# Optimization experiments

Measured on AMD Instinct MI355X. Metric: run time of the kernel, lower is better.

Reference implementation:

```python
import jax, jax.numpy as jnp
import numpy as np

B, N_ANG, LX, LY, LZ = 2, 120, 128, 128, 128


def _rotate_z(vol, phi):
    """Rotate vol [B,Lx,Ly,Lz] by phi radians (counterclockwise) in the (x,y)
    plane about the grid center, bilinear interpolation, zero padding.
    Mirrors pytomography's rotate_detector_z (bilinear grid-sample rotate)."""
    Lx, Ly = vol.shape[1], vol.shape[2]
    dt = vol.dtype
    cx = (Lx - 1) / 2.0
    cy = (Ly - 1) / 2.0
    xs = jnp.arange(Lx, dtype=dt) - cx
    ys = jnp.arange(Ly, dtype=dt) - cy
    X, Y = jnp.meshgrid(xs, ys, indexing="ij")  # [Lx,Ly]
    c, s = jnp.cos(phi), jnp.sin(phi)
    # inverse rotation maps each output pixel to its source location
    sx = c * X + s * Y + cx
    sy = -s * X + c * Y + cy
    x0 = jnp.floor(sx)
    y0 = jnp.floor(sy)
    wx = (sx - x0)[None, :, :, None]
    wy = (sy - y0)[None, :, :, None]
    x0i = x0.astype(jnp.int32)
    y0i = y0.astype(jnp.int32)

    def gather(xi, yi):
        valid = (xi >= 0) & (xi < Lx) & (yi >= 0) & (yi < Ly)
        xic = jnp.clip(xi, 0, Lx - 1)
        yic = jnp.clip(yi, 0, Ly - 1)
        v = vol[:, xic, yic, :]  # [B,Lx,Ly,Lz]
        return v * valid.astype(dt)[None, :, :, None]

    v00 = gather(x0i, y0i)
    v01 = gather(x0i, y0i + 1)
    v10 = gather(x0i + 1, y0i)
    v11 = gather(x0i + 1, y0i + 1)
    return (v00 * (1 - wx) * (1 - wy) + v01 * (1 - wx) * wy
            + v10 * wx * (1 - wy) + v11 * wx * wy)


def setup_inputs() -> dict:
    key = jax.random.key(0)
    image = jax.random.uniform(key, (B, N_ANG, LY, LZ), dtype=jnp.float32)
    angles = jnp.linspace(0.0, 360.0, N_ANG, endpoint=False).astype(jnp.float32)
    return {"image": image, "angles": angles}


def reference(image, angles, delta=1e-11):
    # image: [B, N_angles, Lr, Lz]; angles in degrees.
    Bn, Na, Lr, Lz = image.shape
    Lx = Ly = Lr
    dt = image.dtype
    phis = -jnp.deg2rad(angles).astype(dt)  # negative=True -> back-rotation

    def step(carry, inp):
        obj_acc, norm_acc = carry
        proj, phi = inp  # proj: [B, Lr, Lz]
        # image[:, i].unsqueeze(1) * ones([B, Lx, Ly, Lz]): broadcast along x
        obj_i = jnp.broadcast_to(proj[:, None, :, :], (Bn, Lx, Ly, Lz))
        norm_i = jnp.ones((Bn, Lx, Ly, Lz), dt)
        obj_acc = obj_acc + _rotate_z(obj_i, phi)
        norm_acc = norm_acc + _rotate_z(norm_i, phi)
        return (obj_acc, norm_acc), None

    init = (jnp.zeros((Bn, Lx, Ly, Lz), dt), jnp.zeros((Bn, Lx, Ly, Lz), dt))
    (obj, norm), _ = jax.lax.scan(step, init, (jnp.swapaxes(image, 0, 1), phis))
    return obj / (norm + jnp.asarray(delta, dt))
```

## Files before the change

### kernel.cpp

```cpp
#include <hip/hip_runtime.h>

namespace {

constexpr int L           = 128;
constexpr int NANG        = 120;
constexpr int SLICE_BYTES = L * L * 4;
constexpr int ROW_BYTES   = L * 4;
constexpr int NPTS        = 16;

typedef __fp16 f16x2 __attribute__((ext_vector_type(2)));
typedef __fp16 f16x4 __attribute__((ext_vector_type(4)));
typedef float  f32x4 __attribute__((ext_vector_type(4)));

__global__ __launch_bounds__(512, 8) void bp_kernel(
    const float* __restrict__ image,
    const float* __restrict__ angles,
    float* __restrict__ out)
{
    __shared__ alignas(16) unsigned long long aftab[NANG * 2 * NPTS];
    __shared__ float2   acs[NANG];
    __shared__ unsigned arloB[NANG];
    __shared__ alignas(16) float nrmtab[NPTS];

    const int tid = threadIdx.x;
    const int swz = ((int)blockIdx.x & 7) * 128 + ((int)blockIdx.x >> 3);
    const int yb  = (swz & 31) * 4;
    const int xb  = (swz >> 5) * 4;
    const float cx = (L - 1) * 0.5f;

    if (tid < NANG) {
        const float phi = -angles[tid] * 0.017453292519943295f;
        float s, c;
        sincosf(phi, &s, &c);
        const float X0 = (float)xb - cx,  X1 = (float)(xb + 3) - cx;
        const float Y0 = (float)yb - cx,  Y1 = (float)(yb + 3) - cx;
        const float a00 = -s * X0 + c * Y0 + cx;
        const float a01 = -s * X0 + c * Y1 + cx;
        const float a10 = -s * X1 + c * Y0 + cx;
        const float a11 = -s * X1 + c * Y1 + cx;
        const float symin = fminf(fminf(a00, a01), fminf(a10, a11));
        acs[tid]   = make_float2(c, s);
        arloB[tid] = (unsigned)min(max((int)floorf(symin) - 1, 0), 120) << 9;
    }
    if (tid < NPTS) nrmtab[tid] = 0.f;
    __syncthreads();

    float wsum = 0.f;
#pragma unroll
    for (int k = 0; k < 4; ++k) {
        const int e = tid + k * 512;
        if (e < NANG * NPTS) {
            const int p = e & 15;
            const int a = e >> 4;
            const float2 cs = acs[a];
            const int rlo = (int)(arloB[a] >> 9);
            const float X = (float)(xb + (p >> 2)) - cx;
            const float Y = (float)(yb + (p & 3)) - cx;
            const float sx =  cs.x * X + cs.y * Y + cx;
            const float sy = -cs.y * X + cs.x * Y + cx;
            const float x0f = floorf(sx), y0f = floorf(sy);
            const float wx = sx - x0f,    wy = sy - y0f;
            const int x0 = (int)x0f, y0 = (int)y0f;
            const float mx0 = (x0 >= 0  && x0 <  L)     ? 1.f : 0.f;
            const float mx1 = (x0 >= -1 && x0 <= L - 2) ? 1.f : 0.f;
            const float my0 = (y0 >= 0  && y0 <  L)     ? 1.f : 0.f;
            const float my1 = (y0 >= -1 && y0 <= L - 2) ? 1.f : 0.f;
            const float A   = (1.f - wx) * mx0 + wx * mx1;
            float w0f = (1.f - wy) * my0 * A;
            float w1f = wy * my1 * A;
            const int y0c = min(max(y0, 0), L - 1);
            const int y1c = min(max(y0 + 1, 0), L - 1);
            const int s0  = min(max(y0c - rlo, 0), 7);
            const int s1  = min(max(y1c - rlo, 0), 7);
            if (s0 == s1) { w0f += w1f; w1f = 0.f; }
            f16x2 wh = __builtin_amdgcn_cvt_pkrtz(w0f, w1f);
            const unsigned wbits = *reinterpret_cast<unsigned*>(&wh);
            const unsigned t  = (unsigned)s0 & 3u;
            const int      q0 = s0 >> 2;
            const unsigned long long W = (unsigned long long)wbits << (t * 16u);
            const unsigned long long spill =
                (t == 3u) ? (unsigned long long)(wbits >> 16) : 0ull;
            aftab[a * 32 + p]      = (q0 == 0) ? W : 0ull;
            aftab[a * 32 + 16 + p] = (q0 == 1) ? W : spill;
            wsum += w0f + w1f;
        }
    }
    atomicAdd(&nrmtab[tid & 15], wsum);
    __syncthreads();

    const int wave  = tid >> 6;
    const int lane  = tid & 63;
    const int quad  = lane >> 4;
    const int lhalf = lane & 15;
    const int sel   = quad >> 1;
    const int lq    = quad & 1;
    const int b     = wave & 1;
    const int zq2   = wave >> 1;
    const char* __restrict__ imgc = (const char*)image;

    const unsigned bbase_s = __builtin_amdgcn_readfirstlane((unsigned)(b * NANG) * SLICE_BYTES);
    const unsigned voffc = (unsigned)sel * (unsigned)SLICE_BYTES
                         + (unsigned)(lq * 4) * ROW_BYTES
                         + (unsigned)(zq2 * 32 + 2 * lhalf) * 4u;

    f32x4 acc[2] = {};

    auto read_af = [&](int pr) -> unsigned long long {
        return aftab[pr * 64 + lane];
    };
    auto read_rl = [&](int pr) -> unsigned {
        return arloB[2 * pr + sel];
    };
    auto issue = [&](int pr, unsigned rlB, float2* r) {
        const char* pa = imgc + (bbase_s + ((unsigned)(2 * pr) << 16));
        const unsigned voff = voffc + rlB;
#pragma unroll
        for (int j = 0; j < 4; ++j)
            r[j] = *(const float2*)(pa + (voff + (unsigned)(j * ROW_BYTES)));
    };
    auto compute = [&](unsigned long long afu, const float2* r) {
        union { unsigned long long u; f16x4 v; } c; c.u = afu;
        const f16x2 h0a = __builtin_amdgcn_cvt_pkrtz(r[0].x, r[1].x);
        const f16x2 h0b = __builtin_amdgcn_cvt_pkrtz(r[2].x, r[3].x);
        const f16x2 h1a = __builtin_amdgcn_cvt_pkrtz(r[0].y, r[1].y);
        const f16x2 h1b = __builtin_amdgcn_cvt_pkrtz(r[2].y, r[3].y);
        const f16x4 bf0 = {h0a.x, h0a.y, h0b.x, h0b.y};
        const f16x4 bf1 = {h1a.x, h1a.y, h1b.x, h1b.y};
        acc[0] = __builtin_amdgcn_mfma_f32_16x16x16f16(c.v, bf0, acc[0], 0, 0, 0);
        acc[1] = __builtin_amdgcn_mfma_f32_16x16x16f16(c.v, bf1, acc[1], 0, 0, 0);
    };

    unsigned long long af0, af1, af2;
    unsigned rl0, rl1, rl2;
    float2 rb0[4], rb1[4], rb2[4];

    af0 = read_af(0); rl0 = read_rl(0); issue(0, rl0, rb0);
    af1 = read_af(1); rl1 = read_rl(1); issue(1, rl1, rb1);

    for (int p = 0; p < 60; p += 3) {
        if (p + 2 < 60) { af2 = read_af(p + 2); rl2 = read_rl(p + 2); issue(p + 2, rl2, rb2); }
        compute(af0, rb0);
        if (p + 3 < 60) { af0 = read_af(p + 3); rl0 = read_rl(p + 3); issue(p + 3, rl0, rb0); }
        compute(af1, rb1);
        if (p + 4 < 60) { af1 = read_af(p + 4); rl1 = read_rl(p + 4); issue(p + 4, rl1, rb1); }
        compute(af2, rb2);
    }

    const float4 nrm4 = *(const float4*)&nrmtab[quad * 4];
    const float iv[4] = { 1.f / (nrm4.x + 1e-11f), 1.f / (nrm4.y + 1e-11f),
                          1.f / (nrm4.z + 1e-11f), 1.f / (nrm4.w + 1e-11f) };
    const int zb = zq2 * 32 + 2 * lhalf;
#pragma unroll
    for (int r = 0; r < 4; ++r) {
        const int pnt = quad * 4 + r;
        const int x = xb + (pnt >> 2);
        const int y = yb + (pnt & 3);
        const float2 o = make_float2(acc[0][r] * iv[r], acc[1][r] * iv[r]);
        *reinterpret_cast<float2*>(&out[(((size_t)(b * L + x)) * L + y) * L + zb]) = o;
    }
}

}

extern "C" void kernel_launch(void* const* d_in, const int* in_sizes, int n_in,
                              void* d_out, int out_size, void* d_ws, size_t ws_size,
                              hipStream_t stream) {
    const float* image  = (const float*)d_in[0];
    const float* angles = (const float*)d_in[1];
    float* out = (float*)d_out;
    (void)in_sizes; (void)n_in; (void)out_size; (void)d_ws; (void)ws_size;

    dim3 grid(1024);
    bp_kernel<<<grid, 512, 0, stream>>>(image, angles, out);
}
```

Before: 122.7 us.

## Pre-convert image to fp16 workspace, Morton block order, deeper load pipeline

Adds a pre-pass kernel that converts the fp32 image to fp16 in the workspace, so the main kernel gathers half the bytes and skips the per-iteration fp32-to-fp16 conversions, using byte permutes instead. Block indices are remapped to a Morton (Z-order) tile order to improve L2 locality of rotated reads. The software pipeline depth goes from 3 to 4 buffers. The extra launch and the full image read/write are the added cost, and the fp32 path remains as a fallback when no workspace is available.

```diff
diff --git a/kernel.cpp b/kernel.cpp
--- a/kernel.cpp
+++ b/kernel.cpp
@@ -2,30 +2,52 @@
 
 namespace {
 
-constexpr int L           = 128;
-constexpr int NANG        = 120;
-constexpr int SLICE_BYTES = L * L * 4;
-constexpr int ROW_BYTES   = L * 4;
-constexpr int NPTS        = 16;
+constexpr int L     = 128;
+constexpr int NANG  = 120;
+constexpr int NPTS  = 16;
+constexpr size_t H16_BYTES = (size_t)2 * NANG * L * L * 2;
 
 typedef __fp16 f16x2 __attribute__((ext_vector_type(2)));
 typedef __fp16 f16x4 __attribute__((ext_vector_type(4)));
 typedef float  f32x4 __attribute__((ext_vector_type(4)));
 
+__global__ __launch_bounds__(256) void cvt16_kernel(const float* __restrict__ in,
+                                                    unsigned* __restrict__ out) {
+    const int i = ((int)blockIdx.x * 256 + (int)threadIdx.x) * 4;
+    const float4 v = *reinterpret_cast<const float4*>(in + i);
+    f16x2 a = __builtin_amdgcn_cvt_pkrtz(v.x, v.y);
+    f16x2 b = __builtin_amdgcn_cvt_pkrtz(v.z, v.w);
+    uint2 st;
+    st.x = *reinterpret_cast<unsigned*>(&a);
+    st.y = *reinterpret_cast<unsigned*>(&b);
+    *reinterpret_cast<uint2*>(out + i / 2) = st;
+}
+
+template <bool F16>
 __global__ __launch_bounds__(512, 8) void bp_kernel(
-    const float* __restrict__ image,
+    const void* __restrict__ imgv,
     const float* __restrict__ angles,
     float* __restrict__ out)
 {
+    constexpr unsigned SLICE = F16 ? 32768u : 65536u;
+    constexpr unsigned ROWB  = F16 ? 256u  : 512u;
+    constexpr int      RSH   = F16 ? 8 : 9;
+
     __shared__ alignas(16) unsigned long long aftab[NANG * 2 * NPTS];
     __shared__ float2   acs[NANG];
     __shared__ unsigned arloB[NANG];
     __shared__ alignas(16) float nrmtab[NPTS];
 
     const int tid = threadIdx.x;
-    const int swz = ((int)blockIdx.x & 7) * 128 + ((int)blockIdx.x >> 3);
-    const int yb  = (swz & 31) * 4;
-    const int xb  = (swz >> 5) * 4;
+    const int bid = (int)blockIdx.x;
+    const int n   = ((bid & 7) << 7) | (bid >> 3);
+    int xt = 0, yt = 0;
+#pragma unroll
+    for (int i = 0; i < 5; ++i) {
+        xt |= ((n >> (2 * i)) & 1) << i;
+        yt |= ((n >> (2 * i + 1)) & 1) << i;
+    }
+    const int xb = xt * 4, yb = yt * 4;
     const float cx = (L - 1) * 0.5f;
 
     if (tid < NANG) {
@@ -40,7 +62,7 @@
         const float a11 = -s * X1 + c * Y1 + cx;
         const float symin = fminf(fminf(a00, a01), fminf(a10, a11));
         acs[tid]   = make_float2(c, s);
-        arloB[tid] = (unsigned)min(max((int)floorf(symin) - 1, 0), 120) << 9;
+        arloB[tid] = (unsigned)min(max((int)floorf(symin) - 1, 0), 120) << RSH;
     }
     if (tid < NPTS) nrmtab[tid] = 0.f;
     __syncthreads();
@@ -53,7 +75,7 @@
             const int p = e & 15;
             const int a = e >> 4;
             const float2 cs = acs[a];
-            const int rlo = (int)(arloB[a] >> 9);
+            const int rlo = (int)(arloB[a] >> RSH);
             const float X = (float)(xb + (p >> 2)) - cx;
             const float Y = (float)(yb + (p & 3)) - cx;
             const float sx =  cs.x * X + cs.y * Y + cx;
@@ -96,54 +118,69 @@
     const int lq    = quad & 1;
     const int b     = wave & 1;
     const int zq2   = wave >> 1;
-    const char* __restrict__ imgc = (const char*)image;
-
-    const unsigned bbase_s = __builtin_amdgcn_readfirstlane((unsigned)(b * NANG) * SLICE_BYTES);
-    const unsigned voffc = (unsigned)sel * (unsigned)SLICE_BYTES
-                         + (unsigned)(lq * 4) * ROW_BYTES
-                         + (unsigned)(zq2 * 32 + 2 * lhalf) * 4u;
+    const char* __restrict__ imgc = (const char*)imgv;
+
+    const unsigned bbase_s = __builtin_amdgcn_readfirstlane((unsigned)(b * NANG) * SLICE);
+    const unsigned voffc = (unsigned)sel * SLICE
+                         + (unsigned)(lq * 4) * ROWB
+                         + (unsigned)(zq2 * 32 + 2 * lhalf) * (F16 ? 2u : 4u);
 
     f32x4 acc[2] = {};
 
-    auto read_af = [&](int pr) -> unsigned long long {
-        return aftab[pr * 64 + lane];
+    auto issue = [&](unsigned* r, float2* rfp, unsigned long long& afs, int pr) {
+        afs = aftab[pr * 64 + lane];
+        const unsigned rlB = arloB[2 * pr + sel];
+        const char* pa = imgc + (bbase_s + (unsigned)(2 * pr) * SLICE);
+        const unsigned voff = voffc + rlB;
+        if constexpr (F16) {
+#pragma unroll
+            for (int j = 0; j < 4; ++j)
+                r[j] = *(const unsigned*)(pa + (voff + (unsigned)j * ROWB));
+        } else {
+#pragma unroll
+            for (int j = 0; j < 4; ++j)
+                rfp[j] = *(const float2*)(pa + (voff + (unsigned)j * ROWB));
+        }
     };
-    auto read_rl = [&](int pr) -> unsigned {
-        return arloB[2 * pr + sel];
-    };
-    auto issue = [&](int pr, unsigned rlB, float2* r) {
-        const char* pa = imgc + (bbase_s + ((unsigned)(2 * pr) << 16));
-        const unsigned voff = voffc + rlB;
-#pragma unroll
-        for (int j = 0; j < 4; ++j)
-            r[j] = *(const float2*)(pa + (voff + (unsigned)(j * ROW_BYTES)));
-    };
-    auto compute = [&](unsigned long long afu, const float2* r) {
+    auto compute = [&](const unsigned* r, const float2* rfp, unsigned long long afu) {
         union { unsigned long long u; f16x4 v; } c; c.u = afu;
-        const f16x2 h0a = __builtin_amdgcn_cvt_pkrtz(r[0].x, r[1].x);
-        const f16x2 h0b = __builtin_amdgcn_cvt_pkrtz(r[2].x, r[3].x);
-        const f16x2 h1a = __builtin_amdgcn_cvt_pkrtz(r[0].y, r[1].y);
-        const f16x2 h1b = __builtin_amdgcn_cvt_pkrtz(r[2].y, r[3].y);
-        const f16x4 bf0 = {h0a.x, h0a.y, h0b.x, h0b.y};
-        const f16x4 bf1 = {h1a.x, h1a.y, h1b.x, h1b.y};
+        f16x4 bf0, bf1;
+        if constexpr (F16) {
+            union { unsigned u[2]; f16x4 v; } b0, b1;
+            b0.u[0] = __builtin_amdgcn_perm(r[1], r[0], 0x05040100u);
+            b0.u[1] = __builtin_amdgcn_perm(r[3], r[2], 0x05040100u);
+            b1.u[0] = __builtin_amdgcn_perm(r[1], r[0], 0x07060302u);
+            b1.u[1] = __builtin_amdgcn_perm(r[3], r[2], 0x07060302u);
+            bf0 = b0.v; bf1 = b1.v;
+        } else {
+            const f16x2 h0a = __builtin_amdgcn_cvt_pkrtz(rfp[0].x, rfp[1].x);
+            const f16x2 h0b = __builtin_amdgcn_cvt_pkrtz(rfp[2].x, rfp[3].x);
+            const f16x2 h1a = __builtin_amdgcn_cvt_pkrtz(rfp[0].y, rfp[1].y);
+            const f16x2 h1b = __builtin_amdgcn_cvt_pkrtz(rfp[2].y, rfp[3].y);
+            bf0 = f16x4{h0a.x, h0a.y, h0b.x, h0b.y};
+            bf1 = f16x4{h1a.x, h1a.y, h1b.x, h1b.y};
+        }
         acc[0] = __builtin_amdgcn_mfma_f32_16x16x16f16(c.v, bf0, acc[0], 0, 0, 0);
         acc[1] = __builtin_amdgcn_mfma_f32_16x16x16f16(c.v, bf1, acc[1], 0, 0, 0);
     };
 
-    unsigned long long af0, af1, af2;
-    unsigned rl0, rl1, rl2;
-    float2 rb0[4], rb1[4], rb2[4];
-
-    af0 = read_af(0); rl0 = read_rl(0); issue(0, rl0, rb0);
-    af1 = read_af(1); rl1 = read_rl(1); issue(1, rl1, rb1);
-
-    for (int p = 0; p < 60; p += 3) {
-        if (p + 2 < 60) { af2 = read_af(p + 2); rl2 = read_rl(p + 2); issue(p + 2, rl2, rb2); }
-        compute(af0, rb0);
-        if (p + 3 < 60) { af0 = read_af(p + 3); rl0 = read_rl(p + 3); issue(p + 3, rl0, rb0); }
-        compute(af1, rb1);
-        if (p + 4 < 60) { af1 = read_af(p + 4); rl1 = read_rl(p + 4); issue(p + 4, rl1, rb1); }
-        compute(af2, rb2);
+    unsigned ru0[4], ru1[4], ru2[4], ru3[4];
+    float2   rf0[4], rf1[4], rf2[4], rf3[4];
+    unsigned long long af0, af1, af2, af3;
+
+    issue(ru0, rf0, af0, 0);
+    issue(ru1, rf1, af1, 1);
+    issue(ru2, rf2, af2, 2);
+
+    for (int p = 0; p < 60; p += 4) {
+        if (p + 3 < 60) issue(ru3, rf3, af3, p + 3);
+        compute(ru0, rf0, af0);
+        if (p + 4 < 60) issue(ru0, rf0, af0, p + 4);
+        compute(ru1, rf1, af1);
+        if (p + 5 < 60) issue(ru1, rf1, af1, p + 5);
+        compute(ru2, rf2, af2);
+        if (p + 6 < 60) issue(ru2, rf2, af2, p + 6);
+        compute(ru3, rf3, af3);
     }
 
     const float4 nrm4 = *(const float4*)&nrmtab[quad * 4];
@@ -168,8 +205,13 @@
     const float* image  = (const float*)d_in[0];
     const float* angles = (const float*)d_in[1];
     float* out = (float*)d_out;
-    (void)in_sizes; (void)n_in; (void)out_size; (void)d_ws; (void)ws_size;
+    (void)in_sizes; (void)n_in; (void)out_size;
 
     dim3 grid(1024);
-    bp_kernel<<<grid, 512, 0, stream>>>(image, angles, out);
-}
+    if (d_ws != nullptr && ws_size >= H16_BYTES) {
+        cvt16_kernel<<<dim3(3840), 256, 0, stream>>>(image, (unsigned*)d_ws);
+        bp_kernel<true><<<grid, 512, 0, stream>>>(d_ws, angles, out);
+    } else {
+        bp_kernel<false><<<grid, 512, 0, stream>>>(image, angles, out);
+    }
+}
```

Result: faster. 102.0 us (-16.9%).
